# Kernel optimization log

Measured on AMD Instinct MI355X. Metric: run time of the kernel, lower is better.

Reference implementation:

```python
import jax, jax.numpy as jnp
import numpy as np

H = 8  # hidden size (hardcoded in the module)


def _lstm_scan(x, Wih, Whh, b):
    """Unidirectional LSTM over x:[B,T,I] with PyTorch gate order (i,f,g,o).
    Wih:[4H,I], Whh:[4H,H], b:[4H] (= b_ih + b_hh). Returns h seq [B,T,H]."""
    B = x.shape[0]
    # Precompute input projections for all timesteps in one GEMM: [T,B,4H]
    xg = jnp.einsum('bti,gi->tbg', x, Wih) + b

    def step(carry, xt):
        h, c = carry
        z = xt + h @ Whh.T
        i, f, g, o = jnp.split(z, 4, axis=-1)
        c = jax.nn.sigmoid(f) * c + jax.nn.sigmoid(i) * jnp.tanh(g)
        h = jax.nn.sigmoid(o) * jnp.tanh(c)
        return (h, c), h

    init = (jnp.zeros((B, H), x.dtype), jnp.zeros((B, H), x.dtype))
    _, hs = jax.lax.scan(step, init, xg)  # hs: [T,B,H]
    return jnp.swapaxes(hs, 0, 1)


def _bilstm(x, Wih_f, Whh_f, b_f, Wih_b, Whh_b, b_b):
    fwd = _lstm_scan(x, Wih_f, Whh_f, b_f)
    bwd = _lstm_scan(x[:, ::-1], Wih_b, Whh_b, b_b)[:, ::-1]
    return jnp.concatenate([fwd, bwd], axis=-1)  # [B,T,2H]


def setup_inputs() -> dict:
    key = jax.random.key(0)
    ks = jax.random.split(key, 17)
    s = 1.0 / np.sqrt(H)  # PyTorch uniform(-1/sqrt(H), 1/sqrt(H)) init

    def u(k, shape):
        return jax.random.uniform(k, shape, jnp.float32, -s, s)

    x = jax.random.normal(ks[0], (256, 4096, 8), jnp.float32)
    inp = {'x': x}
    # LSTM params: biases are b_ih + b_hh fused (mathematically identical)
    names = [('Wih1f', (4 * H, 8)), ('Whh1f', (4 * H, H)), ('b1f', (4 * H,)),
             ('Wih1b', (4 * H, 8)), ('Whh1b', (4 * H, H)), ('b1b', (4 * H,)),
             ('Wih2f', (4 * H, 8)), ('Whh2f', (4 * H, H)), ('b2f', (4 * H,)),
             ('Wih2b', (4 * H, 8)), ('Whh2b', (4 * H, H)), ('b2b', (4 * H,)),
             ('W1', (8, 2 * H)), ('bl1', (8,)),
             ('W2', (8, 2 * H)), ('bl2', (8,))]
    for i, (name, shape) in enumerate(names):
        inp[name] = u(ks[i + 1], shape)
    return inp


def reference(x, Wih1f, Whh1f, b1f, Wih1b, Whh1b, b1b,
              Wih2f, Whh2f, b2f, Wih2b, Whh2b, b2b,
              W1, bl1, W2, bl2):
    h1 = _bilstm(x, Wih1f, Whh1f, b1f, Wih1b, Whh1b, b1b)   # [B,T,16]
    y1 = h1 @ W1.T + bl1                                     # [B,T,8]
    h2 = _bilstm(y1, Wih2f, Whh2f, b2f, Wih2b, Whh2b, b2b)  # [B,T,16]
    return h2 @ W2.T + bl2                                   # [B,T,8]
```

## Files before the change

### kernel.cpp

```cpp
#include <hip/hip_runtime.h>

#define T_LEN 4096
#define B_SZ  256

typedef float v2f __attribute__((ext_vector_type(2)));

__device__ __forceinline__ float fexp2(float x) { return __builtin_amdgcn_exp2f(x); }
__device__ __forceinline__ float frcp(float x)  { return __builtin_amdgcn_rcpf(x); }

template<int S>
__device__ __forceinline__ float rorN(float v) {
    return __int_as_float(__builtin_amdgcn_update_dpp(
        0, __float_as_int(v), 0x120 + S, 0xf, 0xf, true));
}

__global__ void init_bias_kernel(const float* __restrict__ bl1,
                                 const float* __restrict__ bl2,
                                 float* __restrict__ y1,
                                 float* __restrict__ out)
{
    const long idx = (long)blockIdx.x * blockDim.x + threadIdx.x;
    float4 a1 = make_float4(bl1[0], bl1[1], bl1[2], bl1[3]);
    float4 b1 = make_float4(bl1[4], bl1[5], bl1[6], bl1[7]);
    float4 a2 = make_float4(bl2[0], bl2[1], bl2[2], bl2[3]);
    float4 b2 = make_float4(bl2[4], bl2[5], bl2[6], bl2[7]);
    float4* y4 = (float4*)y1;
    float4* o4 = (float4*)out;
    y4[idx * 2 + 0] = a1;
    y4[idx * 2 + 1] = b1;
    o4[idx * 2 + 0] = a2;
    o4[idx * 2 + 1] = b2;
}

template<int ST>
__device__ __forceinline__ void rec_body(
    const float* __restrict__ x,
    const float* __restrict__ Wih,
    const float* __restrict__ Whh,
    const float* __restrict__ bias,
    const float* __restrict__ Wp,
    int dcol,
    float* __restrict__ y,
    int b0)
{
    const int tid  = threadIdx.x;
    const int cl   = tid & 15;
    const int j    = cl & 7;
    const int half = cl >> 3;
    const int b    = b0 + (tid >> 4);

    const int rA = half * 16 + j;
    const int rB = half * 16 + 8 + j;

    const float NL2E = -1.4426950408889634f;
    const float GSC  = 2.0f * NL2E;
    const float sA   = half ? GSC : NL2E;
    const float sB   = NL2E;
    const float aselA = half ? 2.0f : 1.0f;
    const float bselA = half ? -1.0f : 0.0f;

    v2f Whk[8], Wik[8];
    float Wcp[8];
    #pragma unroll
    for (int s = 0; s < 8; ++s) {
        const int k = (j - s) & 7;
        Whk[s] = (v2f){Whh[rA * 8 + k] * sA, Whh[rB * 8 + k] * sB};
        Wcp[s] = Wp[j * 16 + dcol + k];
    }
    #pragma unroll
    for (int k = 0; k < 8; ++k)
        Wik[k] = (v2f){Wih[rA * 8 + k] * sA, Wih[rB * 8 + k] * sB};
    const v2f bpk = (v2f){bias[rA] * sA, bias[rB] * sB};

    const int start = (ST > 0) ? 0 : (T_LEN - 1);
    const float* xp = x + ((long)b * T_LEN + start) * 8;
    float*       wp = y + ((long)b * T_LEN + start) * 8 + j;

    float c = 0.0f, h = 0.0f;

    auto step = [&](float4 xa, float4 xb, bool doProj) {
        v2f ip = bpk;
        ip = __builtin_elementwise_fma(Wik[0], (v2f){xa.x, xa.x}, ip);
        ip = __builtin_elementwise_fma(Wik[1], (v2f){xa.y, xa.y}, ip);
        ip = __builtin_elementwise_fma(Wik[2], (v2f){xa.z, xa.z}, ip);
        ip = __builtin_elementwise_fma(Wik[3], (v2f){xa.w, xa.w}, ip);
        ip = __builtin_elementwise_fma(Wik[4], (v2f){xb.x, xb.x}, ip);
        ip = __builtin_elementwise_fma(Wik[5], (v2f){xb.y, xb.y}, ip);
        ip = __builtin_elementwise_fma(Wik[6], (v2f){xb.z, xb.z}, ip);
        ip = __builtin_elementwise_fma(Wik[7], (v2f){xb.w, xb.w}, ip);

        float hr0 = h;
        float hr1 = rorN<1>(h);
        float hr2 = rorN<2>(h);
        float hr3 = rorN<3>(h);
        float hr4 = rorN<4>(h);
        float hr5 = rorN<5>(h);
        float hr6 = rorN<6>(h);
        float hr7 = rorN<7>(h);

        v2f a0 = ip, a1 = {0.0f, 0.0f};
        a0 = __builtin_elementwise_fma(Whk[0], (v2f){hr0, hr0}, a0);
        a1 = __builtin_elementwise_fma(Whk[1], (v2f){hr1, hr1}, a1);
        a0 = __builtin_elementwise_fma(Whk[2], (v2f){hr2, hr2}, a0);
        a1 = __builtin_elementwise_fma(Whk[3], (v2f){hr3, hr3}, a1);
        a0 = __builtin_elementwise_fma(Whk[4], (v2f){hr4, hr4}, a0);
        a1 = __builtin_elementwise_fma(Whk[5], (v2f){hr5, hr5}, a1);
        a0 = __builtin_elementwise_fma(Whk[6], (v2f){hr6, hr6}, a0);
        a1 = __builtin_elementwise_fma(Whk[7], (v2f){hr7, hr7}, a1);
        const v2f z = a0 + a1;

        if (doProj) {
            float pa = hr0 * Wcp[0];
            pa = fmaf(hr1, Wcp[1], pa);
            pa = fmaf(hr2, Wcp[2], pa);
            pa = fmaf(hr3, Wcp[3], pa);
            pa = fmaf(hr4, Wcp[4], pa);
            pa = fmaf(hr5, Wcp[5], pa);
            pa = fmaf(hr6, Wcp[6], pa);
            pa = fmaf(hr7, Wcp[7], pa);
            if ((tid & 8) == 0) atomicAdd(wp, pa);
            wp += ST * 8;
        }

        const float vA = fmaf(frcp(1.0f + fexp2(z.x)), aselA, bselA);
        const float vB = frcp(1.0f + fexp2(z.y));

        const float pAx = rorN<8>(vA);
        const float pBx = rorN<8>(vB);
        const float gi = half ? pAx : vA;
        const float gf = half ? pBx : vB;
        const float gg = half ? vA  : pAx;
        const float go = half ? vB  : pBx;

        c = fmaf(gf, c, gi * gg);
        const float th = fmaf(frcp(1.0f + fexp2(c * GSC)), 2.0f, -1.0f);
        h = go * th;
    };

    float4 A0, A1, A2, A3, A4, A5, A6, A7;
    float4 B0, B1, B2, B3, B4, B5, B6, B7;
    float4 C0, C1, C2, C3, C4, C5, C6, C7;

#define LOADM(P0, P1, P2, P3, P4, P5, P6, P7)                                  \
    P0 = *(const float4*)(xp);                                                 \
    P1 = *(const float4*)(xp + 4);                                             \
    P2 = *(const float4*)(xp + ST * 8);                                        \
    P3 = *(const float4*)(xp + ST * 8 + 4);                                    \
    P4 = *(const float4*)(xp + ST * 16);                                       \
    P5 = *(const float4*)(xp + ST * 16 + 4);                                   \
    P6 = *(const float4*)(xp + ST * 24);                                       \
    P7 = *(const float4*)(xp + ST * 24 + 4);                                   \
    xp += ST * 32;                                                             \
    __builtin_amdgcn_sched_barrier(0);

#define MACRO4(P0, P1, P2, P3, P4, P5, P6, P7, FIRSTPROJ)                      \
    step(P0, P1, FIRSTPROJ);                                                   \
    step(P2, P3, true);                                                        \
    step(P4, P5, true);                                                        \
    step(P6, P7, true);

    LOADM(A0, A1, A2, A3, A4, A5, A6, A7)
    LOADM(B0, B1, B2, B3, B4, B5, B6, B7)
    LOADM(C0, C1, C2, C3, C4, C5, C6, C7)
    MACRO4(A0, A1, A2, A3, A4, A5, A6, A7, false)

    for (int i = 0; i < 340; ++i) {
        LOADM(A0, A1, A2, A3, A4, A5, A6, A7)
        MACRO4(B0, B1, B2, B3, B4, B5, B6, B7, true)
        LOADM(B0, B1, B2, B3, B4, B5, B6, B7)
        MACRO4(C0, C1, C2, C3, C4, C5, C6, C7, true)
        LOADM(C0, C1, C2, C3, C4, C5, C6, C7)
        MACRO4(A0, A1, A2, A3, A4, A5, A6, A7, true)
    }
    LOADM(A0, A1, A2, A3, A4, A5, A6, A7)
    MACRO4(B0, B1, B2, B3, B4, B5, B6, B7, true)
    MACRO4(C0, C1, C2, C3, C4, C5, C6, C7, true)
    MACRO4(A0, A1, A2, A3, A4, A5, A6, A7, true)

#undef LOADM
#undef MACRO4

    {
        float pa = h * Wcp[0];
        pa = fmaf(rorN<1>(h), Wcp[1], pa);
        pa = fmaf(rorN<2>(h), Wcp[2], pa);
        pa = fmaf(rorN<3>(h), Wcp[3], pa);
        pa = fmaf(rorN<4>(h), Wcp[4], pa);
        pa = fmaf(rorN<5>(h), Wcp[5], pa);
        pa = fmaf(rorN<6>(h), Wcp[6], pa);
        pa = fmaf(rorN<7>(h), Wcp[7], pa);
        if ((tid & 8) == 0) atomicAdd(wp, pa);
    }
}

__global__ __launch_bounds__(64, 1)
void lstm_rec_kernel(const float* __restrict__ x,
                     const float* __restrict__ WihF, const float* __restrict__ WhhF,
                     const float* __restrict__ bF,
                     const float* __restrict__ WihB, const float* __restrict__ WhhB,
                     const float* __restrict__ bB,
                     const float* __restrict__ Wp,
                     float* __restrict__ y)
{
    if (blockIdx.x < 64)
        rec_body<1 >(x, WihF, WhhF, bF, Wp, 0, y, 4 * (int)blockIdx.x);
    else
        rec_body<-1>(x, WihB, WhhB, bB, Wp, 8, y, 4 * ((int)blockIdx.x - 64));
}

extern "C" void kernel_launch(void* const* d_in, const int* in_sizes, int n_in,
                              void* d_out, int out_size, void* d_ws, size_t ws_size,
                              hipStream_t stream)
{
    const float* x     = (const float*)d_in[0];
    const float* Wih1f = (const float*)d_in[1];
    const float* Whh1f = (const float*)d_in[2];
    const float* b1f   = (const float*)d_in[3];
    const float* Wih1b = (const float*)d_in[4];
    const float* Whh1b = (const float*)d_in[5];
    const float* b1b   = (const float*)d_in[6];
    const float* Wih2f = (const float*)d_in[7];
    const float* Whh2f = (const float*)d_in[8];
    const float* b2f   = (const float*)d_in[9];
    const float* Wih2b = (const float*)d_in[10];
    const float* Whh2b = (const float*)d_in[11];
    const float* b2b   = (const float*)d_in[12];
    const float* W1    = (const float*)d_in[13];
    const float* bl1   = (const float*)d_in[14];
    const float* W2    = (const float*)d_in[15];
    const float* bl2   = (const float*)d_in[16];

    float* out = (float*)d_out;
    float* y1  = (float*)d_ws;

    const int BT = B_SZ * T_LEN;

    init_bias_kernel<<<BT / 256, 256, 0, stream>>>(bl1, bl2, y1, out);

    lstm_rec_kernel<<<128, 64, 0, stream>>>(x, Wih1f, Whh1f, b1f,
                                            Wih1b, Whh1b, b1b, W1, y1);

    lstm_rec_kernel<<<128, 64, 0, stream>>>(y1, Wih2f, Whh2f, b2f,
                                            Wih2b, Whh2b, b2b, W2, out);
}
```

Before: 1.315 ms.

## Hand-schedule x prefetch with inline asm loads and explicit vmcnt waits

Replaces the compiler-generated float4 loads with inline-asm global_load_dwordx4 that use immediate offsets. Explicit s_waitcnt vmcnt counts let the triple-buffered prefetch keep several batches of loads in flight instead of the compiler inserting conservative waits. The projection atomic is now issued by all 16 lanes without the branch, with the projection weights halved so the two duplicate adds sum to the same value. This removes lane-divergence control flow, at the cost of twice the atomic traffic and fragile hand-counted vmcnt values. Because the atomics also increment vmcnt, a wrong count could expose loaded data before it is ready.

```diff
diff --git a/kernel.cpp b/kernel.cpp
--- a/kernel.cpp
+++ b/kernel.cpp
@@ -4,6 +4,7 @@
 #define B_SZ  256
 
 typedef float v2f __attribute__((ext_vector_type(2)));
+typedef float v4f __attribute__((ext_vector_type(4)));
 
 __device__ __forceinline__ float fexp2(float x) { return __builtin_amdgcn_exp2f(x); }
 __device__ __forceinline__ float frcp(float x)  { return __builtin_amdgcn_rcpf(x); }
@@ -12,6 +13,18 @@
 __device__ __forceinline__ float rorN(float v) {
     return __int_as_float(__builtin_amdgcn_update_dpp(
         0, __float_as_int(v), 0x120 + S, 0xf, 0xf, true));
+}
+
+template<int OFF>
+__device__ __forceinline__ v4f aload(const float* p) {
+    v4f r;
+    asm volatile("global_load_dwordx4 %0, %1, off offset:%2"
+                 : "=v"(r) : "v"(p), "i"(OFF) : "memory");
+    return r;
+}
+__device__ __forceinline__ void aatomic(float* p, float v) {
+    asm volatile("global_atomic_add_f32 %0, %1, off"
+                 :: "v"(p), "v"(v) : "memory");
 }
 
 __global__ void init_bias_kernel(const float* __restrict__ bl1,
@@ -34,13 +47,13 @@
 
 template<int ST>
 __device__ __forceinline__ void rec_body(
-    const float* __restrict__ x,
-    const float* __restrict__ Wih,
-    const float* __restrict__ Whh,
-    const float* __restrict__ bias,
-    const float* __restrict__ Wp,
+    const float* x,
+    const float* Wih,
+    const float* Whh,
+    const float* bias,
+    const float* Wp,
     int dcol,
-    float* __restrict__ y,
+    float* y,
     int b0)
 {
     const int tid  = threadIdx.x;
@@ -65,7 +78,7 @@
     for (int s = 0; s < 8; ++s) {
         const int k = (j - s) & 7;
         Whk[s] = (v2f){Whh[rA * 8 + k] * sA, Whh[rB * 8 + k] * sB};
-        Wcp[s] = Wp[j * 16 + dcol + k];
+        Wcp[s] = Wp[j * 16 + dcol + k] * 0.5f;
     }
     #pragma unroll
     for (int k = 0; k < 8; ++k)
@@ -78,7 +91,7 @@
 
     float c = 0.0f, h = 0.0f;
 
-    auto step = [&](float4 xa, float4 xb, bool doProj) {
+    auto step = [&](v4f xa, v4f xb, bool doProj) {
         v2f ip = bpk;
         ip = __builtin_elementwise_fma(Wik[0], (v2f){xa.x, xa.x}, ip);
         ip = __builtin_elementwise_fma(Wik[1], (v2f){xa.y, xa.y}, ip);
@@ -118,7 +131,7 @@
             pa = fmaf(hr5, Wcp[5], pa);
             pa = fmaf(hr6, Wcp[6], pa);
             pa = fmaf(hr7, Wcp[7], pa);
-            if ((tid & 8) == 0) atomicAdd(wp, pa);
+            aatomic(wp, pa);
             wp += ST * 8;
         }
 
@@ -137,48 +150,67 @@
         h = go * th;
     };
 
-    float4 A0, A1, A2, A3, A4, A5, A6, A7;
-    float4 B0, B1, B2, B3, B4, B5, B6, B7;
-    float4 C0, C1, C2, C3, C4, C5, C6, C7;
-
-#define LOADM(P0, P1, P2, P3, P4, P5, P6, P7)                                  \
-    P0 = *(const float4*)(xp);                                                 \
-    P1 = *(const float4*)(xp + 4);                                             \
-    P2 = *(const float4*)(xp + ST * 8);                                        \
-    P3 = *(const float4*)(xp + ST * 8 + 4);                                    \
-    P4 = *(const float4*)(xp + ST * 16);                                       \
-    P5 = *(const float4*)(xp + ST * 16 + 4);                                   \
-    P6 = *(const float4*)(xp + ST * 24);                                       \
-    P7 = *(const float4*)(xp + ST * 24 + 4);                                   \
-    xp += ST * 32;                                                             \
-    __builtin_amdgcn_sched_barrier(0);
-
-#define MACRO4(P0, P1, P2, P3, P4, P5, P6, P7, FIRSTPROJ)                      \
+    v4f A0, A1, A2, A3, A4, A5, A6, A7;
+    v4f B0, B1, B2, B3, B4, B5, B6, B7;
+    v4f C0, C1, C2, C3, C4, C5, C6, C7;
+
+#define AREGS A0, A1, A2, A3, A4, A5, A6, A7
+#define BREGS B0, B1, B2, B3, B4, B5, B6, B7
+#define CREGS C0, C1, C2, C3, C4, C5, C6, C7
+
+#define LOADM_I(P0, P1, P2, P3, P4, P5, P6, P7)                                \
+    P0 = aload<0>(xp);            P1 = aload<16>(xp);                          \
+    P2 = aload<ST * 32>(xp);      P3 = aload<ST * 32 + 16>(xp);                \
+    P4 = aload<ST * 64>(xp);      P5 = aload<ST * 64 + 16>(xp);                \
+    P6 = aload<ST * 96>(xp);      P7 = aload<ST * 96 + 16>(xp);                \
+    xp += ST * 32;
+#define LOADM(REGS) LOADM_I(REGS)
+
+#define WAITM_I(N, P0, P1, P2, P3, P4, P5, P6, P7)                             \
+    asm volatile("s_waitcnt vmcnt(" #N ")"                                     \
+        : "+v"(P0), "+v"(P1), "+v"(P2), "+v"(P3),                              \
+          "+v"(P4), "+v"(P5), "+v"(P6), "+v"(P7) :: "memory")
+#define WAITM(N, REGS) WAITM_I(N, REGS)
+
+#define MACRO4_I(P0, P1, P2, P3, P4, P5, P6, P7, FIRSTPROJ)                    \
     step(P0, P1, FIRSTPROJ);                                                   \
     step(P2, P3, true);                                                        \
     step(P4, P5, true);                                                        \
     step(P6, P7, true);
-
-    LOADM(A0, A1, A2, A3, A4, A5, A6, A7)
-    LOADM(B0, B1, B2, B3, B4, B5, B6, B7)
-    LOADM(C0, C1, C2, C3, C4, C5, C6, C7)
-    MACRO4(A0, A1, A2, A3, A4, A5, A6, A7, false)
-
-    for (int i = 0; i < 340; ++i) {
-        LOADM(A0, A1, A2, A3, A4, A5, A6, A7)
-        MACRO4(B0, B1, B2, B3, B4, B5, B6, B7, true)
-        LOADM(B0, B1, B2, B3, B4, B5, B6, B7)
-        MACRO4(C0, C1, C2, C3, C4, C5, C6, C7, true)
-        LOADM(C0, C1, C2, C3, C4, C5, C6, C7)
-        MACRO4(A0, A1, A2, A3, A4, A5, A6, A7, true)
+#define MACRO4(REGS, FIRSTPROJ) MACRO4_I(REGS, FIRSTPROJ)
+
+    asm volatile("s_waitcnt vmcnt(0)" ::: "memory");
+
+    LOADM(AREGS)
+    LOADM(BREGS)
+    LOADM(CREGS)
+    WAITM(16, AREGS); MACRO4(AREGS, false)
+    LOADM(AREGS)
+    WAITM(19, BREGS); MACRO4(BREGS, true)
+    LOADM(BREGS)
+    WAITM(23, CREGS); MACRO4(CREGS, true)
+
+    for (int i = 0; i < 339; ++i) {
+        LOADM(CREGS) WAITM(24, AREGS); MACRO4(AREGS, true)
+        LOADM(AREGS) WAITM(24, BREGS); MACRO4(BREGS, true)
+        LOADM(BREGS) WAITM(24, CREGS); MACRO4(CREGS, true)
     }
-    LOADM(A0, A1, A2, A3, A4, A5, A6, A7)
-    MACRO4(B0, B1, B2, B3, B4, B5, B6, B7, true)
-    MACRO4(C0, C1, C2, C3, C4, C5, C6, C7, true)
-    MACRO4(A0, A1, A2, A3, A4, A5, A6, A7, true)
+    LOADM(CREGS)
+    WAITM(24, AREGS); MACRO4(AREGS, true)
+    LOADM(AREGS)
+    WAITM(24, BREGS); MACRO4(BREGS, true)
+    WAITM(16, CREGS); MACRO4(CREGS, true)
+    WAITM(8,  AREGS); MACRO4(AREGS, true)
 
 #undef LOADM
+#undef LOADM_I
 #undef MACRO4
+#undef MACRO4_I
+#undef WAITM
+#undef WAITM_I
+#undef AREGS
+#undef BREGS
+#undef CREGS
 
     {
         float pa = h * Wcp[0];
@@ -189,7 +221,7 @@
         pa = fmaf(rorN<5>(h), Wcp[5], pa);
         pa = fmaf(rorN<6>(h), Wcp[6], pa);
         pa = fmaf(rorN<7>(h), Wcp[7], pa);
-        if ((tid & 8) == 0) atomicAdd(wp, pa);
+        aatomic(wp, pa);
     }
 }
 
```

Measured after the change: 1.099 ms. -16.5%, faster.
